# Kernel tuning notes

Hardware: AMD Instinct MI355X
Metric: run time of the kernel (lower is better)

The kernel has to match this reference:

```python
import jax, jax.numpy as jnp
import numpy as np

# Module config (init_kwargs)
CIN, COUT, KH, KW = 256, 256, 3, 3
STRIDE, PADDING = 1, 1
T = 64                 # psum chunk size along the reduction (K) axis
NBITS = 8              # saturating accumulator bits (signed)
QMAX = (1 << (NBITS - 1)) - 1   # 127
QMIN = QMAX - (1 << NBITS) + 1  # -128


def setup_inputs() -> dict:
    key = jax.random.key(0)
    k1, k2 = jax.random.split(key)
    x = jax.random.normal(k1, (8, CIN, 56, 56), dtype=jnp.float32)
    # nn.Parameter(torch.rand((N,1)) * 0.001)
    weights = jax.random.uniform(k2, (CIN * COUT * KH * KW, 1), dtype=jnp.float32) * 0.001
    return {"x": x, "weights": weights}


def reference(x, weights):
    B, _, H, W = x.shape
    OH = (H - KH + 2 * PADDING) // STRIDE + 1
    OW = (W - KW + 2 * PADDING) // STRIDE + 1

    w = weights.reshape(COUT, CIN, KH, KW)
    # per-output-channel scaling factor, detached
    scale = jax.lax.stop_gradient(jnp.mean(jnp.abs(w), axis=(1, 2, 3), keepdims=True))
    # binarize with STE: sign(w).detach() - clamp(w).detach() + clamp(w)
    wc = jnp.clip(w, -1.0, 1.0)
    wb = jax.lax.stop_gradient(jnp.sign(w) - wc) + wc

    # unfold (im2col); channel varies slowest -> matches torch.nn.functional.unfold
    patches = jax.lax.conv_general_dilated_patches(
        x, (KH, KW), (STRIDE, STRIDE), [(PADDING, PADDING), (PADDING, PADDING)]
    )  # [B, CIN*KH*KW, OH*OW... (spatial)]
    K = CIN * KH * KW
    L = OH * OW
    A = patches.reshape(B, K, L).transpose(0, 2, 1)  # [B, L, K]
    X = wb.reshape(COUT, K).T                        # [K, COUT]

    pad = (-K) % T
    if pad:
        A = jnp.pad(A, ((0, 0), (0, 0), (0, pad)))
        X = jnp.pad(X, ((0, pad), (0, 0)))
    nT = (K + pad) // T

    A4 = A.reshape(B, L, nT, T)        # chunked reduction axis
    X3 = X.reshape(nT, T, COUT)
    # per-chunk partial sums (satmm_cuda.forward_psum)
    psum = jnp.einsum('blnt,ntc->nblc', A4, X3)  # [nT, B, L, COUT]

    # saturating sequential accumulation: reduce(lambda a,b: clip(a+b, QMIN, QMAX))
    def step(carry, p):
        return jnp.clip(carry + p, QMIN, QMAX), None
    y_flat, _ = jax.lax.scan(step, psum[0], psum[1:])  # [B, L, COUT]

    y = y_flat.transpose(0, 2, 1).reshape(B, COUT, OH, OW)
    y = y * scale.reshape(1, -1, 1, 1)
    # psum returned in the original [B, L, COUT, nT] layout
    return y, psum.transpose(1, 2, 3, 0)
```

## Files before the change

### kernel.cpp

```cpp
#include <hip/hip_runtime.h>
#include <hip/hip_bf16.h>

#define CIN 256
#define COUT 256
#define HW 56
#define BATCH 8
#define L_SPATIAL 3136
#define K_TOTAL 2304
#define NT 36
#define KSTRIDE 2312
#define ATILE_BYTES (16 * KSTRIDE * 2)
#define STAGE_FLOATS 2304
#define LDS_BYTES (ATILE_BYTES + 8 * STAGE_FLOATS * 4)
#define TILES_PER_IMG 196
#define QMAXF 127.0f
#define QMINF -128.0f

typedef short bf16x8 __attribute__((ext_vector_type(8)));
typedef float f32x4 __attribute__((ext_vector_type(4)));

__device__ __forceinline__ void nt_store4(float* p, f32x4 v) {
  __builtin_nontemporal_store(v, reinterpret_cast<f32x4*>(p));
}

__global__ __launch_bounds__(256) void prep_kernel(
    const float* __restrict__ w, unsigned short* __restrict__ bsign,
    float* __restrict__ scale) {
  const int c = blockIdx.x;
  const int t = threadIdx.x;
  const float* row = w + (size_t)c * K_TOTAL;
  unsigned short* out = bsign + (size_t)c * K_TOTAL;
  float acc = 0.0f;
#pragma unroll
  for (int j = 0; j < 9; ++j) {
    const int k = t + 256 * j;
    const float v = row[k];
    acc += __builtin_fabsf(v);
    out[k] = (v > 0.0f) ? (unsigned short)0x3F80
           : ((v < 0.0f) ? (unsigned short)0xBF80 : (unsigned short)0);
  }
#pragma unroll
  for (int o = 32; o > 0; o >>= 1) acc += __shfl_down(acc, o, 64);
  __shared__ float red[4];
  if ((t & 63) == 0) red[t >> 6] = acc;
  __syncthreads();
  if (t == 0) scale[c] = (red[0] + red[1] + red[2] + red[3]) * (1.0f / 2304.0f);
}

__global__ __launch_bounds__(512, 1) void satconv_kernel(
    const float* __restrict__ x, const unsigned short* __restrict__ bsign,
    const float* __restrict__ scale, float* __restrict__ y_out,
    float* __restrict__ psum_out) {
  extern __shared__ char smem[];
  unsigned short* Atile = (unsigned short*)smem;
  float* stage_base = (float*)(smem + ATILE_BYTES);

  const int tid = threadIdx.x;
  const int m_tile = (blockIdx.x & 7) * TILES_PER_IMG + (blockIdx.x >> 3);
  const int m0 = m_tile << 4;

  {
    const int ml = tid & 15;
    const int grp = tid >> 4;
    const int m = m0 + ml;
    const int b = m / L_SPATIAL;
    const int l = m - b * L_SPATIAL;
    const int oh = l / HW;
    const int ow = l - oh * HW;
    const float* xb = x + (size_t)b * (CIN * L_SPATIAL);
    unsigned short* arow = Atile + ml * KSTRIDE;
    for (int r = grp; r < 768; r += 32) {
      const int ci = r / 3;
      const int kh = r - ci * 3;
      const int h = oh + kh - 1;
      const bool hv = ((unsigned)h < (unsigned)HW);
      const float* xr = xb + (ci * HW + h) * HW;
      const int kb = ci * 9 + kh * 3;
#pragma unroll
      for (int kw = 0; kw < 3; ++kw) {
        const int wv = ow + kw - 1;
        float v = 0.0f;
        if (hv && ((unsigned)wv < (unsigned)HW)) v = xr[wv];
        __hip_bfloat16 bv = __float2bfloat16(v);
        arow[kb + kw] = *reinterpret_cast<unsigned short*>(&bv);
      }
    }
  }

  const int lane = tid & 63;
  const int wave = tid >> 6;
  const int cl = lane & 15;
  const int q = lane >> 4;
  const int c0 = wave << 5;
  float* stage = stage_base + wave * STAGE_FLOATS;

  const float sc_s0 = scale[c0 + cl];
  const float sc_s1 = scale[c0 + 16 + cl];

  int base_it[9];
  {
#pragma unroll
    for (int it = 0; it < 9; ++it) {
      const int f = it * 256 + lane * 4;
      const int qq = f / 576;
      const int rem = f - qq * 576;
      const int ci = rem / 36;
      const int n0 = rem - ci * 36;
      base_it[it] = ((m0 + (qq << 2)) * COUT + ci) * NT + n0;
    }
  }

  __syncthreads();

  const unsigned short* aptr = Atile + cl * KSTRIDE + q * 8;
  const int b_img = m0 / L_SPATIAL;
  const int l0 = m0 - b_img * L_SPATIAL;

  for (int s = 0; s < 2; ++s) {
    const int csub0 = c0 + (s << 4);
    const int c = csub0 + cl;
    const unsigned short* bptr = bsign + (size_t)c * K_TOTAL + q * 8;
    f32x4 ps[NT];
    f32x4 sacc = {0.0f, 0.0f, 0.0f, 0.0f};
    const f32x4 zero = {0.0f, 0.0f, 0.0f, 0.0f};
    bf16x8 b0 = *reinterpret_cast<const bf16x8*>(bptr);
    bf16x8 b1 = *reinterpret_cast<const bf16x8*>(bptr + 32);
#pragma unroll
    for (int n = 0; n < NT; ++n) {
      bf16x8 nb0, nb1;
      if (n + 1 < NT) {
        nb0 = *reinterpret_cast<const bf16x8*>(bptr + (n + 1) * 64);
        nb1 = *reinterpret_cast<const bf16x8*>(bptr + (n + 1) * 64 + 32);
      }
      bf16x8 a0 = *reinterpret_cast<const bf16x8*>(aptr + n * 64);
      bf16x8 a1 = *reinterpret_cast<const bf16x8*>(aptr + n * 64 + 32);
      f32x4 acc = __builtin_amdgcn_mfma_f32_16x16x32_bf16(a0, b0, zero, 0, 0, 0);
      acc = __builtin_amdgcn_mfma_f32_16x16x32_bf16(a1, b1, acc, 0, 0, 0);
      ps[n] = acc;
      if (n == 0) {
        sacc = acc;
      } else {
#pragma unroll
        for (int e = 0; e < 4; ++e) {
          const float t = sacc[e] + acc[e];
          sacc[e] = __builtin_amdgcn_fmed3f(t, QMINF, QMAXF);
        }
      }
      b0 = nb0;
      b1 = nb1;
    }

    {
      const float sc = (s == 0) ? sc_s0 : sc_s1;
      f32x4 yv;
#pragma unroll
      for (int e = 0; e < 4; ++e) yv[e] = sacc[e] * sc;
      *reinterpret_cast<f32x4*>(stage + cl * 16 + q * 4) = yv;
      const int ci = lane >> 2;
      const int mi = (lane & 3) << 2;
      f32x4 v = *reinterpret_cast<const f32x4*>(stage + lane * 4);
      nt_store4(y_out + ((size_t)b_img * COUT + (csub0 + ci)) * L_SPATIAL + l0 + mi, v);
    }

    const int soff = csub0 * NT;
#pragma unroll
    for (int rg = 0; rg < 4; ++rg) {
#pragma unroll
      for (int g = 0; g < 9; ++g) {
        f32x4 v = {ps[4 * g + 0][rg], ps[4 * g + 1][rg],
                   ps[4 * g + 2][rg], ps[4 * g + 3][rg]};
        *reinterpret_cast<f32x4*>(stage + q * 576 + cl * 36 + 4 * g) = v;
      }
      const int rgoff = rg * (COUT * NT) + soff;
#pragma unroll
      for (int it = 0; it < 9; ++it) {
        f32x4 v = *reinterpret_cast<const f32x4*>(stage + it * 256 + lane * 4);
        nt_store4(psum_out + (size_t)(base_it[it] + rgoff), v);
      }
    }
  }
}

extern "C" void kernel_launch(void* const* d_in, const int* in_sizes, int n_in,
                              void* d_out, int out_size, void* d_ws, size_t ws_size,
                              hipStream_t stream) {
  const float* x = (const float*)d_in[0];
  const float* w = (const float*)d_in[1];
  float* y = (float*)d_out;
  float* psum = y + (size_t)BATCH * COUT * L_SPATIAL;
  unsigned short* bsign = (unsigned short*)d_ws;
  float* scale = (float*)((char*)d_ws + (size_t)COUT * K_TOTAL * 2);

  prep_kernel<<<COUT, 256, 0, stream>>>(w, bsign, scale);

  hipFuncSetAttribute(reinterpret_cast<const void*>(satconv_kernel),
                      hipFuncAttributeMaxDynamicSharedMemorySize, LDS_BYTES);
  satconv_kernel<<<(BATCH * L_SPATIAL) / 16, 512, LDS_BYTES, stream>>>(
      x, bsign, scale, y, psum);
}
```

Before: 1.186 ms.

## Store psum directly from registers, drop LDS staging, raise occupancy

Removes the per-wave LDS staging buffer and writes each group of four psum chunks straight from MFMA results to global memory as 16-byte stores. The y output is likewise stored directly, without transposing through LDS. The smaller LDS footprint and launch bounds of (512,4) allow more blocks per CU, and the B-operand prefetch becomes a three-deep ring. Writes are now less coalesced: each lane touches a separate row segment and the non-temporal hint on psum is gone. Register pressure under the tighter launch bounds could cause spills.

```diff
diff --git a/kernel.cpp b/kernel.cpp
--- a/kernel.cpp
+++ b/kernel.cpp
@@ -8,10 +8,10 @@
 #define L_SPATIAL 3136
 #define K_TOTAL 2304
 #define NT 36
+#define ROWF (COUT * NT)
 #define KSTRIDE 2312
 #define ATILE_BYTES (16 * KSTRIDE * 2)
-#define STAGE_FLOATS 2304
-#define LDS_BYTES (ATILE_BYTES + 8 * STAGE_FLOATS * 4)
+#define LDS_BYTES ATILE_BYTES
 #define TILES_PER_IMG 196
 #define QMAXF 127.0f
 #define QMINF -128.0f
@@ -47,13 +47,12 @@
   if (t == 0) scale[c] = (red[0] + red[1] + red[2] + red[3]) * (1.0f / 2304.0f);
 }
 
-__global__ __launch_bounds__(512, 1) void satconv_kernel(
+__global__ __launch_bounds__(512, 4) void satconv_kernel(
     const float* __restrict__ x, const unsigned short* __restrict__ bsign,
     const float* __restrict__ scale, float* __restrict__ y_out,
     float* __restrict__ psum_out) {
   extern __shared__ char smem[];
   unsigned short* Atile = (unsigned short*)smem;
-  float* stage_base = (float*)(smem + ATILE_BYTES);
 
   const int tid = threadIdx.x;
   const int m_tile = (blockIdx.x & 7) * TILES_PER_IMG + (blockIdx.x >> 3);
@@ -92,23 +91,9 @@
   const int cl = lane & 15;
   const int q = lane >> 4;
   const int c0 = wave << 5;
-  float* stage = stage_base + wave * STAGE_FLOATS;
 
   const float sc_s0 = scale[c0 + cl];
   const float sc_s1 = scale[c0 + 16 + cl];
-
-  int base_it[9];
-  {
-#pragma unroll
-    for (int it = 0; it < 9; ++it) {
-      const int f = it * 256 + lane * 4;
-      const int qq = f / 576;
-      const int rem = f - qq * 576;
-      const int ci = rem / 36;
-      const int n0 = rem - ci * 36;
-      base_it[it] = ((m0 + (qq << 2)) * COUT + ci) * NT + n0;
-    }
-  }
 
   __syncthreads();
 
@@ -116,68 +101,64 @@
   const int b_img = m0 / L_SPATIAL;
   const int l0 = m0 - b_img * L_SPATIAL;
 
+#pragma unroll
   for (int s = 0; s < 2; ++s) {
-    const int csub0 = c0 + (s << 4);
-    const int c = csub0 + cl;
-    const unsigned short* bptr = bsign + (size_t)c * K_TOTAL + q * 8;
-    f32x4 ps[NT];
-    f32x4 sacc = {0.0f, 0.0f, 0.0f, 0.0f};
+    const int c = c0 + (s << 4) + cl;
+    const unsigned short* bp = bsign + (size_t)c * K_TOTAL + q * 8;
+    float* pb0 = psum_out + (size_t)(m0 + (q << 2)) * ROWF + c * NT;
+    float* pb1 = pb0 + ROWF;
+    float* pb2 = pb0 + 2 * ROWF;
+    float* pb3 = pb0 + 3 * ROWF;
+    const float sc = (s == 0) ? sc_s0 : sc_s1;
+
+    bf16x8 b0[3], b1[3];
+    b0[0] = *reinterpret_cast<const bf16x8*>(bp);
+    b1[0] = *reinterpret_cast<const bf16x8*>(bp + 32);
+    b0[1] = *reinterpret_cast<const bf16x8*>(bp + 64);
+    b1[1] = *reinterpret_cast<const bf16x8*>(bp + 96);
+
     const f32x4 zero = {0.0f, 0.0f, 0.0f, 0.0f};
-    bf16x8 b0 = *reinterpret_cast<const bf16x8*>(bptr);
-    bf16x8 b1 = *reinterpret_cast<const bf16x8*>(bptr + 32);
+    f32x4 sacc = zero;
+
 #pragma unroll
-    for (int n = 0; n < NT; ++n) {
-      bf16x8 nb0, nb1;
-      if (n + 1 < NT) {
-        nb0 = *reinterpret_cast<const bf16x8*>(bptr + (n + 1) * 64);
-        nb1 = *reinterpret_cast<const bf16x8*>(bptr + (n + 1) * 64 + 32);
-      }
-      bf16x8 a0 = *reinterpret_cast<const bf16x8*>(aptr + n * 64);
-      bf16x8 a1 = *reinterpret_cast<const bf16x8*>(aptr + n * 64 + 32);
-      f32x4 acc = __builtin_amdgcn_mfma_f32_16x16x32_bf16(a0, b0, zero, 0, 0, 0);
-      acc = __builtin_amdgcn_mfma_f32_16x16x32_bf16(a1, b1, acc, 0, 0, 0);
-      ps[n] = acc;
-      if (n == 0) {
-        sacc = acc;
-      } else {
+    for (int g = 0; g < 9; ++g) {
+      f32x4 pch[4];
 #pragma unroll
-        for (int e = 0; e < 4; ++e) {
-          const float t = sacc[e] + acc[e];
-          sacc[e] = __builtin_amdgcn_fmed3f(t, QMINF, QMAXF);
+      for (int j = 0; j < 4; ++j) {
+        const int n = 4 * g + j;
+        if (n + 2 < NT) {
+          b0[(n + 2) % 3] = *reinterpret_cast<const bf16x8*>(bp + (n + 2) * 64);
+          b1[(n + 2) % 3] = *reinterpret_cast<const bf16x8*>(bp + (n + 2) * 64 + 32);
+        }
+        bf16x8 a0 = *reinterpret_cast<const bf16x8*>(aptr + n * 64);
+        bf16x8 a1 = *reinterpret_cast<const bf16x8*>(aptr + n * 64 + 32);
+        f32x4 acc = __builtin_amdgcn_mfma_f32_16x16x32_bf16(a0, b0[n % 3], zero, 0, 0, 0);
+        acc = __builtin_amdgcn_mfma_f32_16x16x32_bf16(a1, b1[n % 3], acc, 0, 0, 0);
+        pch[j] = acc;
+        if (n == 0) {
+          sacc = acc;
+        } else {
+#pragma unroll
+          for (int e = 0; e < 4; ++e) {
+            const float t = sacc[e] + acc[e];
+            sacc[e] = __builtin_amdgcn_fmed3f(t, QMINF, QMAXF);
+          }
         }
       }
-      b0 = nb0;
-      b1 = nb1;
+      f32x4 v0 = {pch[0][0], pch[1][0], pch[2][0], pch[3][0]};
+      f32x4 v1 = {pch[0][1], pch[1][1], pch[2][1], pch[3][1]};
+      f32x4 v2 = {pch[0][2], pch[1][2], pch[2][2], pch[3][2]};
+      f32x4 v3 = {pch[0][3], pch[1][3], pch[2][3], pch[3][3]};
+      *reinterpret_cast<f32x4*>(pb0 + 4 * g) = v0;
+      *reinterpret_cast<f32x4*>(pb1 + 4 * g) = v1;
+      *reinterpret_cast<f32x4*>(pb2 + 4 * g) = v2;
+      *reinterpret_cast<f32x4*>(pb3 + 4 * g) = v3;
     }
 
-    {
-      const float sc = (s == 0) ? sc_s0 : sc_s1;
-      f32x4 yv;
+    f32x4 yv;
 #pragma unroll
-      for (int e = 0; e < 4; ++e) yv[e] = sacc[e] * sc;
-      *reinterpret_cast<f32x4*>(stage + cl * 16 + q * 4) = yv;
-      const int ci = lane >> 2;
-      const int mi = (lane & 3) << 2;
-      f32x4 v = *reinterpret_cast<const f32x4*>(stage + lane * 4);
-      nt_store4(y_out + ((size_t)b_img * COUT + (csub0 + ci)) * L_SPATIAL + l0 + mi, v);
-    }
-
-    const int soff = csub0 * NT;
-#pragma unroll
-    for (int rg = 0; rg < 4; ++rg) {
-#pragma unroll
-      for (int g = 0; g < 9; ++g) {
-        f32x4 v = {ps[4 * g + 0][rg], ps[4 * g + 1][rg],
-                   ps[4 * g + 2][rg], ps[4 * g + 3][rg]};
-        *reinterpret_cast<f32x4*>(stage + q * 576 + cl * 36 + 4 * g) = v;
-      }
-      const int rgoff = rg * (COUT * NT) + soff;
-#pragma unroll
-      for (int it = 0; it < 9; ++it) {
-        f32x4 v = *reinterpret_cast<const f32x4*>(stage + it * 256 + lane * 4);
-        nt_store4(psum_out + (size_t)(base_it[it] + rgoff), v);
-      }
-    }
+    for (int e = 0; e < 4; ++e) yv[e] = sacc[e] * sc;
+    nt_store4(y_out + ((size_t)b_img * COUT + c) * L_SPATIAL + l0 + (q << 2), yv);
   }
 }
 
```

Result: slower. 1.910 ms (+61.0%).

## Split output channels across blocks and halve per-wave psum registers

Applied to the files above, without the earlier changes.

Each block now covers 64 output channels instead of 256, so there are four times as many blocks. Each pair of waves recomputes the full saturating chain but keeps only half of the 36 partial-sum chunks in registers. The A-tile LDS is reused as the staging buffer for transposing psum, which allows higher occupancy (launch bounds 512,4). The cost is that the im2col A tile is rebuilt four times per M tile and the MFMA work is doubled by the redundant half-chains. In exchange, register pressure drops, LDS per block shrinks, and latency hiding improves.

```diff
diff --git a/kernel.cpp b/kernel.cpp
--- a/kernel.cpp
+++ b/kernel.cpp
@@ -8,10 +8,12 @@
 #define L_SPATIAL 3136
 #define K_TOTAL 2304
 #define NT 36
+#define NH 18
+#define ROWF (COUT * NT)
 #define KSTRIDE 2312
 #define ATILE_BYTES (16 * KSTRIDE * 2)
-#define STAGE_FLOATS 2304
-#define LDS_BYTES (ATILE_BYTES + 8 * STAGE_FLOATS * 4)
+#define LDS_BYTES ATILE_BYTES
+#define MT_TOTAL 1568
 #define TILES_PER_IMG 196
 #define QMAXF 127.0f
 #define QMINF -128.0f
@@ -47,16 +49,51 @@
   if (t == 0) scale[c] = (red[0] + red[1] + red[2] + red[3]) * (1.0f / 2304.0f);
 }
 
-__global__ __launch_bounds__(512, 1) void satconv_kernel(
+template <int H>
+__device__ __forceinline__ void compute_half(
+    const unsigned short* __restrict__ aptr,
+    const unsigned short* __restrict__ bptr,
+    f32x4* __restrict__ ps, f32x4& sacc) {
+  const f32x4 zero = {0.0f, 0.0f, 0.0f, 0.0f};
+  bf16x8 b0 = *reinterpret_cast<const bf16x8*>(bptr);
+  bf16x8 b1 = *reinterpret_cast<const bf16x8*>(bptr + 32);
+#pragma unroll
+  for (int n = 0; n < NT; ++n) {
+    bf16x8 nb0, nb1;
+    if (n + 1 < NT) {
+      nb0 = *reinterpret_cast<const bf16x8*>(bptr + (n + 1) * 64);
+      nb1 = *reinterpret_cast<const bf16x8*>(bptr + (n + 1) * 64 + 32);
+    }
+    bf16x8 a0 = *reinterpret_cast<const bf16x8*>(aptr + n * 64);
+    bf16x8 a1 = *reinterpret_cast<const bf16x8*>(aptr + n * 64 + 32);
+    f32x4 acc = __builtin_amdgcn_mfma_f32_16x16x32_bf16(a0, b0, zero, 0, 0, 0);
+    acc = __builtin_amdgcn_mfma_f32_16x16x32_bf16(a1, b1, acc, 0, 0, 0);
+    if (n >= H * NH && n < (H + 1) * NH) ps[n - H * NH] = acc;
+    if (n == 0) {
+      sacc = acc;
+    } else {
+#pragma unroll
+      for (int e = 0; e < 4; ++e)
+        sacc[e] = __builtin_amdgcn_fmed3f(sacc[e] + acc[e], QMINF, QMAXF);
+    }
+    b0 = nb0;
+    b1 = nb1;
+  }
+}
+
+__global__ __launch_bounds__(512, 4) void satconv_kernel(
     const float* __restrict__ x, const unsigned short* __restrict__ bsign,
     const float* __restrict__ scale, float* __restrict__ y_out,
     float* __restrict__ psum_out) {
   extern __shared__ char smem[];
   unsigned short* Atile = (unsigned short*)smem;
-  float* stage_base = (float*)(smem + ATILE_BYTES);
+  float* stage = (float*)smem;
 
   const int tid = threadIdx.x;
-  const int m_tile = (blockIdx.x & 7) * TILES_PER_IMG + (blockIdx.x >> 3);
+  const int bid = blockIdx.x;
+  const int mt = bid % MT_TOTAL;
+  const int cb = bid / MT_TOTAL;
+  const int m_tile = (mt & 7) * TILES_PER_IMG + (mt >> 3);
   const int m0 = m_tile << 4;
 
   {
@@ -91,93 +128,63 @@
   const int wave = tid >> 6;
   const int cl = lane & 15;
   const int q = lane >> 4;
-  const int c0 = wave << 5;
-  float* stage = stage_base + wave * STAGE_FLOATS;
-
-  const float sc_s0 = scale[c0 + cl];
-  const float sc_s1 = scale[c0 + 16 + cl];
-
-  int base_it[9];
-  {
-#pragma unroll
-    for (int it = 0; it < 9; ++it) {
-      const int f = it * 256 + lane * 4;
-      const int qq = f / 576;
-      const int rem = f - qq * 576;
-      const int ci = rem / 36;
-      const int n0 = rem - ci * 36;
-      base_it[it] = ((m0 + (qq << 2)) * COUT + ci) * NT + n0;
-    }
-  }
+  const int cs = wave >> 1;
+  const int h = wave & 1;
+  const int c = (cb << 6) + (cs << 4) + cl;
+
+  const float sc = scale[c];
 
   __syncthreads();
 
   const unsigned short* aptr = Atile + cl * KSTRIDE + q * 8;
+  const unsigned short* bptr = bsign + (size_t)c * K_TOTAL + q * 8;
   const int b_img = m0 / L_SPATIAL;
   const int l0 = m0 - b_img * L_SPATIAL;
 
-  for (int s = 0; s < 2; ++s) {
-    const int csub0 = c0 + (s << 4);
-    const int c = csub0 + cl;
-    const unsigned short* bptr = bsign + (size_t)c * K_TOTAL + q * 8;
-    f32x4 ps[NT];
-    f32x4 sacc = {0.0f, 0.0f, 0.0f, 0.0f};
-    const f32x4 zero = {0.0f, 0.0f, 0.0f, 0.0f};
-    bf16x8 b0 = *reinterpret_cast<const bf16x8*>(bptr);
-    bf16x8 b1 = *reinterpret_cast<const bf16x8*>(bptr + 32);
-#pragma unroll
-    for (int n = 0; n < NT; ++n) {
-      bf16x8 nb0, nb1;
-      if (n + 1 < NT) {
-        nb0 = *reinterpret_cast<const bf16x8*>(bptr + (n + 1) * 64);
-        nb1 = *reinterpret_cast<const bf16x8*>(bptr + (n + 1) * 64 + 32);
+  f32x4 ps[NH];
+  f32x4 sacc;
+  if (h == 0) compute_half<0>(aptr, bptr, ps, sacc);
+  else        compute_half<1>(aptr, bptr, ps, sacc);
+
+  if (h == 0) {
+    f32x4 yv;
+#pragma unroll
+    for (int e = 0; e < 4; ++e) yv[e] = sacc[e] * sc;
+    nt_store4(y_out + ((size_t)b_img * COUT + c) * L_SPATIAL + l0 + (q << 2), yv);
+  }
+
+  __syncthreads();
+
+#pragma unroll
+  for (int r = 0; r < 2; ++r) {
+    if ((cs >> 1) == r) {
+      float* reg = stage + (cs & 1) * 9216;
+      const int coldw = cl * 36 + h * NH;
+#pragma unroll
+      for (int j = 0; j < NH; ++j) {
+#pragma unroll
+        for (int e = 0; e < 4; ++e)
+          reg[((q << 2) + e) * 576 + coldw + j] = ps[j][e];
       }
-      bf16x8 a0 = *reinterpret_cast<const bf16x8*>(aptr + n * 64);
-      bf16x8 a1 = *reinterpret_cast<const bf16x8*>(aptr + n * 64 + 32);
-      f32x4 acc = __builtin_amdgcn_mfma_f32_16x16x32_bf16(a0, b0, zero, 0, 0, 0);
-      acc = __builtin_amdgcn_mfma_f32_16x16x32_bf16(a1, b1, acc, 0, 0, 0);
-      ps[n] = acc;
-      if (n == 0) {
-        sacc = acc;
-      } else {
-#pragma unroll
-        for (int e = 0; e < 4; ++e) {
-          const float t = sacc[e] + acc[e];
-          sacc[e] = __builtin_amdgcn_fmed3f(t, QMINF, QMAXF);
-        }
+    }
+    __syncthreads();
+    {
+      const int CS = wave >> 2;
+      const int mrow0 = (wave & 3) << 2;
+      const int cs_g = (r << 1) + CS;
+      const float* lds_f = stage + wave * 2304;
+      float* gbase = psum_out + (size_t)(m0 + mrow0) * ROWF
+                   + ((cb << 6) + (cs_g << 4)) * 36;
+#pragma unroll
+      for (int i = 0; i < 9; ++i) {
+        const int xx = i * 256 + (lane << 2);
+        const int ml = xx / 576;
+        const int roff = xx - ml * 576;
+        f32x4 v = *reinterpret_cast<const f32x4*>(lds_f + xx);
+        nt_store4(gbase + (size_t)ml * ROWF + roff, v);
       }
-      b0 = nb0;
-      b1 = nb1;
-    }
-
-    {
-      const float sc = (s == 0) ? sc_s0 : sc_s1;
-      f32x4 yv;
-#pragma unroll
-      for (int e = 0; e < 4; ++e) yv[e] = sacc[e] * sc;
-      *reinterpret_cast<f32x4*>(stage + cl * 16 + q * 4) = yv;
-      const int ci = lane >> 2;
-      const int mi = (lane & 3) << 2;
-      f32x4 v = *reinterpret_cast<const f32x4*>(stage + lane * 4);
-      nt_store4(y_out + ((size_t)b_img * COUT + (csub0 + ci)) * L_SPATIAL + l0 + mi, v);
-    }
-
-    const int soff = csub0 * NT;
-#pragma unroll
-    for (int rg = 0; rg < 4; ++rg) {
-#pragma unroll
-      for (int g = 0; g < 9; ++g) {
-        f32x4 v = {ps[4 * g + 0][rg], ps[4 * g + 1][rg],
-                   ps[4 * g + 2][rg], ps[4 * g + 3][rg]};
-        *reinterpret_cast<f32x4*>(stage + q * 576 + cl * 36 + 4 * g) = v;
-      }
-      const int rgoff = rg * (COUT * NT) + soff;
-#pragma unroll
-      for (int it = 0; it < 9; ++it) {
-        f32x4 v = *reinterpret_cast<const f32x4*>(stage + it * 256 + lane * 4);
-        nt_store4(psum_out + (size_t)(base_it[it] + rgoff), v);
-      }
-    }
+    }
+    __syncthreads();
   }
 }
 
@@ -195,6 +202,6 @@
 
   hipFuncSetAttribute(reinterpret_cast<const void*>(satconv_kernel),
                       hipFuncAttributeMaxDynamicSharedMemorySize, LDS_BYTES);
-  satconv_kernel<<<(BATCH * L_SPATIAL) / 16, 512, LDS_BYTES, stream>>>(
+  satconv_kernel<<<MT_TOTAL * 4, 512, LDS_BYTES, stream>>>(
       x, bsign, scale, y, psum);
 }
```

New measurement: 1.430 ms. +20.5%, slower.
